# Kernel tuning notes

Hardware: AMD Instinct MI355X
Metric: run time of the kernel (lower is better)

Reference implementation:

```python
import jax, jax.numpy as jnp
import numpy as np

B, N, D, H = 4, 16384, 256, 2
EPS_LN = 1e-5
EPS_NORM = 1e-12


def _layernorm(x, w, b):
    # WithBias_LayerNorm over last dim (biased variance)
    mu = jnp.mean(x, axis=-1, keepdims=True)
    var = jnp.var(x, axis=-1, keepdims=True)
    return (x - mu) / jnp.sqrt(var + EPS_LN) * w + b


def _l2norm(x):
    # torch F.normalize along dim=-1
    n = jnp.sqrt(jnp.sum(x * x, axis=-1, keepdims=True))
    return x / jnp.maximum(n, EPS_NORM)


def setup_inputs() -> dict:
    key = jax.random.key(0)
    ks = jax.random.split(key, 8)
    s = 0.02
    return {
        "input_R": jax.random.normal(ks[0], (B, N, D), jnp.float32),
        "input_S": jax.random.normal(ks[1], (B, N, D), jnp.float32),
        "lnS_w": jnp.ones((D,), jnp.float32),
        "lnS_b": jnp.zeros((D,), jnp.float32),
        "lnR_w": jnp.ones((D,), jnp.float32),
        "lnR_b": jnp.zeros((D,), jnp.float32),
        "Wq": jax.random.normal(ks[2], (D, D), jnp.float32) * s,
        "bq": jax.random.normal(ks[3], (D,), jnp.float32) * s,
        "Wkv": jax.random.normal(ks[4], (2 * D, D), jnp.float32) * s,
        "bkv": jax.random.normal(ks[5], (2 * D,), jnp.float32) * s,
        "Wo": jax.random.normal(ks[6], (D, D), jnp.float32) * s,
        "bo": jax.random.normal(ks[7], (D,), jnp.float32) * s,
        "temperature": jnp.ones((H, 1, 1), jnp.float32),
    }


def reference(input_R, input_S, lnS_w, lnS_b, lnR_w, lnR_b,
              Wq, bq, Wkv, bkv, Wo, bo, temperature):
    b, n, d = input_S.shape
    h = temperature.shape[0]
    c = d // h
    # LayerNorm over channels, then permute to [b, d, n] (Conv1d layout)
    x = _layernorm(input_R, lnR_w, lnR_b).transpose(0, 2, 1)  # kv source
    y = _layernorm(input_S, lnS_w, lnS_b).transpose(0, 2, 1)  # q source
    # 1x1 conv == channel matmul
    kv = jnp.einsum('od,bdn->bon', Wkv, x) + bkv[None, :, None]  # [b,2d,n]
    k, v = jnp.split(kv, 2, axis=1)                              # [b,d,n]
    q = jnp.einsum('od,bdn->bon', Wq, y) + bq[None, :, None]     # [b,d,n]
    # split heads: [b, h, c, n]
    q = _l2norm(q.reshape(b, h, c, n))
    k = _l2norm(k.reshape(b, h, c, n))
    v = v.reshape(b, h, c, n)
    # channel attention: [b,h,c,c]
    attn = jnp.einsum('bhcn,bhdn->bhcd', q, k) * temperature[None]
    attn = jax.nn.softmax(attn, axis=-1)
    out = jnp.einsum('bhcd,bhdn->bhcn', attn, v).reshape(b, d, n)
    out = jnp.einsum('od,bdn->bon', Wo, out) + bo[None, :, None]
    return out.transpose(0, 2, 1)  # [b, n, d]
```

## Files before the change

### kernel.cpp

```cpp
#include <hip/hip_runtime.h>
#include <hip/hip_bf16.h>

typedef __attribute__((ext_vector_type(8))) short short8;
typedef __attribute__((ext_vector_type(4))) float f32x4;
typedef unsigned short u16;

#define DEVI static __device__ __forceinline__

constexpr int kB = 4;
constexpr int kN = 16384;
constexpr int kD = 256;
constexpr int kH = 2;
constexpr int kC = 128;

constexpr size_t SZ_T16 = (size_t)kB * kD * kN * 2;
constexpr size_t O_Yt   = 0;
constexpr size_t O_Xt   = O_Yt + SZ_T16;
constexpr size_t O_Xrow = O_Xt + SZ_T16;
constexpr size_t SZ_G   = (size_t)3 * kB * kD * kD * 4;
constexpr size_t O_G    = O_Xrow + SZ_T16;
constexpr size_t O_ysum = O_G + SZ_G;
constexpr size_t O_xsum = O_ysum + (size_t)kB * kD * 4;
constexpr size_t O_T    = O_xsum + (size_t)kB * kD * 4;
constexpr size_t O_qy   = O_T + SZ_G;
constexpr size_t O_kq   = O_qy + (size_t)kB * kD * 4;
constexpr size_t O_nq2  = O_kq + (size_t)kB * kD * 4;
constexpr size_t O_nk2  = O_nq2 + (size_t)kB * kD * 4;
constexpr size_t O_A    = O_nk2 + (size_t)kB * kD * 4;
constexpr size_t SZ_A   = (size_t)kB * kH * kC * kC * 4;
constexpr size_t O_W3   = O_A + SZ_A;
constexpr size_t O_b3   = O_W3 + (size_t)kB * kD * kD * 2;
constexpr size_t WS_NEED = O_b3 + (size_t)kB * kD * 4;

DEVI u16 f2bf(float x) {
    unsigned u = __builtin_bit_cast(unsigned, x);
    unsigned r = (u + 0x7FFFu + ((u >> 16) & 1u)) >> 16;
    return (u16)r;
}

DEVI void gload_lds16(const void* g, void* l) {
    __builtin_amdgcn_global_load_lds(
        (const __attribute__((address_space(1))) unsigned int*)g,
        (__attribute__((address_space(3))) unsigned int*)l, 16, 0, 0);
}

__global__ __launch_bounds__(256) void ln_kernel(
    const float* __restrict__ x, const float* __restrict__ w, const float* __restrict__ bia,
    u16* __restrict__ outT, u16* __restrict__ outR, float* __restrict__ colsum)
{
    constexpr int ROWS = 32;
    __shared__ u16 tile[256][36];
    __shared__ float csum[4][256];
    int blk = blockIdx.x;
    int b = blk >> 9;
    int n0 = (blk & 511) * ROWS;
    int lane = threadIdx.x & 63, wave = threadIdx.x >> 6;

    float wv[4], bv[4];
#pragma unroll
    for (int j = 0; j < 4; j++) { int c = lane + 64 * j; wv[j] = w[c]; bv[j] = bia[c]; }
    float acc[4] = {0.f, 0.f, 0.f, 0.f};

    for (int i = 0; i < 8; i++) {
        int r = wave * 8 + i;
        const float* xp = x + ((size_t)(b * kN + n0 + r)) * kD;
        float v[4];
#pragma unroll
        for (int j = 0; j < 4; j++) v[j] = xp[lane + 64 * j];
        float s  = v[0] + v[1] + v[2] + v[3];
        float sq = v[0]*v[0] + v[1]*v[1] + v[2]*v[2] + v[3]*v[3];
#pragma unroll
        for (int off = 32; off; off >>= 1) { s += __shfl_xor(s, off); sq += __shfl_xor(sq, off); }
        float mean = s * (1.f / kD);
        float var  = sq * (1.f / kD) - mean * mean;
        float rstd = rsqrtf(var + 1e-5f);
#pragma unroll
        for (int j = 0; j < 4; j++) {
            float y = (v[j] - mean) * rstd * wv[j] + bv[j];
            acc[j] += y;
            u16 u = f2bf(y);
            tile[lane + 64 * j][r] = u;
            if (outR) outR[((size_t)(b * kN + n0 + r)) * kD + lane + 64 * j] = u;
        }
    }
#pragma unroll
    for (int j = 0; j < 4; j++) csum[wave][lane + 64 * j] = acc[j];
    __syncthreads();
    int t = threadIdx.x;
    unsafeAtomicAdd(&colsum[b * kD + t], csum[0][t] + csum[1][t] + csum[2][t] + csum[3][t]);

#pragma unroll
    for (int pass = 0; pass < 2; pass++) {
        int c = pass * 128 + (t >> 1);
        int q = t & 1;
        const u16* src = &tile[c][q * 16];
        uint2 p0 = *(const uint2*)(src + 0);
        uint2 p1 = *(const uint2*)(src + 4);
        uint2 p2 = *(const uint2*)(src + 8);
        uint2 p3 = *(const uint2*)(src + 12);
        u16* dst = outT + ((size_t)(b * kD + c)) * kN + n0 + q * 16;
        *(uint4*)(dst)     = make_uint4(p0.x, p0.y, p1.x, p1.y);
        *(uint4*)(dst + 8) = make_uint4(p2.x, p2.y, p3.x, p3.y);
    }
}

__global__ __launch_bounds__(256) void gram_kernel(
    const u16* __restrict__ Yt, const u16* __restrict__ Xt, float* __restrict__ G)
{
    __shared__ __align__(16) char smem[32768];

    int id = blockIdx.x;
    int b = id / 192;
    int r = id % 192;
    int chunk = r / 12;
    int r2 = r % 12;
    int which = r2 >> 2;
    int tm = (r2 >> 1) & 1, tn = r2 & 1;
    const u16* Ap = (which == 2) ? Xt : Yt;
    const u16* Bp = (which == 1) ? Yt : Xt;

    int lane = threadIdx.x & 63, wave = threadIdx.x >> 6;
    int wr = wave >> 1, wc = wave & 1;
    int li = lane & 15, klo = lane >> 4;

    const u16* Abase = Ap + ((size_t)(b * kD + tm * 128)) * kN + (size_t)chunk * 1024;
    const u16* Bbase = Bp + ((size_t)(b * kD + tn * 128)) * kN + (size_t)chunk * 1024;
    const u16* gsrcA[4];
    const u16* gsrcB[4];
    char* ldst[4];
#pragma unroll
    for (int j = 0; j < 4; j++) {
        int u = (wave * 4 + j) * 64 + lane;
        int row = u >> 3;
        int sl = ((u & 7) ^ (row & 7)) * 8;
        gsrcA[j] = Abase + (size_t)row * kN + sl;
        gsrcB[j] = Bbase + (size_t)row * kN + sl;
        ldst[j] = smem + (wave * 4 + j) * 1024;
    }

    unsigned offA[2][4], offB[2][4];
#pragma unroll
    for (int kk = 0; kk < 2; kk++)
#pragma unroll
        for (int f = 0; f < 4; f++) {
            int rowA = wr * 64 + f * 16 + li;
            int rowB = wc * 64 + f * 16 + li;
            int e = kk * 32 + klo * 8;
            offA[kk][f] = rowA * 128 + ((e ^ ((rowA & 7) << 3)) * 2);
            offB[kk][f] = 16384 + rowB * 128 + ((e ^ ((rowB & 7) << 3)) * 2);
        }

    f32x4 acc[4][4] = {};
    for (int step = 0; step < 16; step++) {
#pragma unroll
        for (int j = 0; j < 4; j++) {
            gload_lds16(gsrcA[j] + step * 64, ldst[j]);
            gload_lds16(gsrcB[j] + step * 64, ldst[j] + 16384);
        }
        __syncthreads();
#pragma unroll
        for (int kk = 0; kk < 2; kk++) {
            short8 a[4], bb[4];
#pragma unroll
            for (int f = 0; f < 4; f++) a[f]  = *(const short8*)(smem + offA[kk][f]);
#pragma unroll
            for (int f = 0; f < 4; f++) bb[f] = *(const short8*)(smem + offB[kk][f]);
#pragma unroll
            for (int fi = 0; fi < 4; fi++)
#pragma unroll
                for (int fj = 0; fj < 4; fj++)
                    acc[fi][fj] = __builtin_amdgcn_mfma_f32_16x16x32_bf16(a[fi], bb[fj], acc[fi][fj], 0, 0, 0);
        }
        __syncthreads();
    }

    float* Gb = G + ((size_t)(which * 4 + b)) * (kD * kD);
#pragma unroll
    for (int fi = 0; fi < 4; fi++) {
        int row = tm * 128 + wr * 64 + fi * 16 + klo * 4;
#pragma unroll
        for (int fj = 0; fj < 4; fj++) {
            int col = tn * 128 + wc * 64 + fj * 16 + li;
#pragma unroll
            for (int rr = 0; rr < 4; rr++)
                unsafeAtomicAdd(&Gb[(size_t)(row + rr) * kD + col], acc[fi][fj][rr]);
        }
    }
}

__global__ __launch_bounds__(256) void tmul_kernel(
    const float* __restrict__ G, const float* __restrict__ Wq, const float* __restrict__ Wkv,
    float* __restrict__ T)
{
    int id = blockIdx.x;
    int otile = id & 31; id >>= 5;
    int b = id & 3;      id >>= 2;
    int which = id;
    const float* W  = (which == 2) ? Wkv : Wq;
    const float* Gb = G + ((size_t)(which * 4 + b)) * (kD * kD);
    float* Tb       = T + ((size_t)(which * 4 + b)) * (kD * kD);
    int d = threadIdx.x;
    int o0 = otile * 8;
    float acc[8] = {};
    for (int m = 0; m < 256; m++) {
        float g = Gb[(size_t)m * kD + d];
#pragma unroll
        for (int oo = 0; oo < 8; oo++) acc[oo] = fmaf(W[(o0 + oo) * kD + m], g, acc[oo]);
    }
#pragma unroll
    for (int oo = 0; oo < 8; oo++) Tb[(size_t)(o0 + oo) * kD + d] = acc[oo];
}

__global__ __launch_bounds__(256) void vec_kernel(
    const float* __restrict__ T, const float* __restrict__ Wq, const float* __restrict__ Wkv,
    const float* __restrict__ bq, const float* __restrict__ bkv,
    const float* __restrict__ ysum, const float* __restrict__ xsum,
    float* __restrict__ qy, float* __restrict__ kq,
    float* __restrict__ nq2, float* __restrict__ nk2)
{
    __shared__ float ys[256], xs[256];
    int b = blockIdx.x, e = threadIdx.x;
    ys[e] = ysum[b * kD + e];
    xs[e] = xsum[b * kD + e];
    __syncthreads();
    const float* T2  = T + ((size_t)(1 * 4 + b)) * (kD * kD) + (size_t)e * kD;
    const float* T3  = T + ((size_t)(2 * 4 + b)) * (kD * kD) + (size_t)e * kD;
    const float* wqr = Wq + (size_t)e * kD;
    const float* wkr = Wkv + (size_t)e * kD;
    float dqy = 0, dkq = 0, d2 = 0, d3 = 0;
    for (int m = 0; m < 256; m++) {
        float a = wqr[m], c = wkr[m];
        dqy = fmaf(a, ys[m], dqy);
        dkq = fmaf(c, xs[m], dkq);
        d2  = fmaf(T2[m], a, d2);
        d3  = fmaf(T3[m], c, d3);
    }
    float bqe = bq[e], bke = bkv[e];
    qy[b * kD + e] = dqy;
    kq[b * kD + e] = dkq;
    nq2[b * kD + e] = d2 + 2.f * bqe * dqy + (float)kN * bqe * bqe;
    nk2[b * kD + e] = d3 + 2.f * bke * dkq + (float)kN * bke * bke;
}

__global__ __launch_bounds__(128) void attn_kernel(
    const float* __restrict__ T, const float* __restrict__ Wkv,
    const float* __restrict__ bq, const float* __restrict__ bkv,
    const float* __restrict__ qy, const float* __restrict__ kq,
    const float* __restrict__ nq2, const float* __restrict__ nk2,
    const float* __restrict__ temperature, float* __restrict__ A)
{
    __shared__ float t1[256];
    __shared__ float red[4];
    int id = blockIdx.x;
    int c = id & 127; id >>= 7;
    int h = id & 1;
    int b = id >> 1;
    int e = h * 128 + c;
    int d = threadIdx.x;

    const float* T1 = T + ((size_t)(0 * 4 + b)) * (kD * kD) + (size_t)e * kD;
    t1[d] = T1[d];
    t1[128 + d] = T1[128 + d];
    __syncthreads();

    int f = h * 128 + d;
    const float* wkr = Wkv + (size_t)f * kD;
    float acc = 0;
    for (int m = 0; m < 256; m++) acc = fmaf(t1[m], wkr[m], acc);

    float bqe = bq[e], bkf = bkv[f];
    float graw = acc + bqe * kq[b * kD + f] + bkf * qy[b * kD + e] + (float)kN * bqe * bkf;
    float rq = 1.f / fmaxf(sqrtf(fmaxf(nq2[b * kD + e], 0.f)), 1e-12f);
    float rk = 1.f / fmaxf(sqrtf(fmaxf(nk2[b * kD + f], 0.f)), 1e-12f);
    float logit = graw * rq * rk * temperature[h];

    float mx = logit;
#pragma unroll
    for (int off = 32; off; off >>= 1) mx = fmaxf(mx, __shfl_xor(mx, off));
    int wv = d >> 6;
    if ((d & 63) == 0) red[wv] = mx;
    __syncthreads();
    mx = fmaxf(red[0], red[1]);
    float p = __expf(logit - mx);
    float sm = p;
#pragma unroll
    for (int off = 32; off; off >>= 1) sm += __shfl_xor(sm, off);
    if ((d & 63) == 0) red[2 + wv] = sm;
    __syncthreads();
    sm = red[2] + red[3];
    A[((size_t)((b * 2 + h) * kC + c)) * kC + d] = p / sm;
}

__global__ __launch_bounds__(256) void mmat_kernel(
    const float* __restrict__ A, const float* __restrict__ Wo,
    const float* __restrict__ Wkv, const float* __restrict__ bkv,
    const float* __restrict__ bo, u16* __restrict__ W3, float* __restrict__ b3)
{
    __shared__ float Ml[256];
    int id = blockIdx.x;
    int o = id & 255;
    int b = id >> 8;
    int t = threadIdx.x;
    int h = t >> 7, d = t & 127;

    const float* Ab  = A + ((size_t)(b * 2 + h)) * (kC * kC);
    const float* wor = Wo + (size_t)o * kD + h * 128;
    float acc = 0;
    for (int c2 = 0; c2 < 128; c2++) acc = fmaf(wor[c2], Ab[(size_t)c2 * kC + d], acc);
    Ml[t] = acc;
    __syncthreads();

    const float* wvp = Wkv + (size_t)256 * kD;
    float w3 = 0, bsum = 0;
    for (int e2 = 0; e2 < 256; e2++) {
        float m = Ml[e2];
        w3   = fmaf(m, wvp[(size_t)e2 * kD + t], w3);
        bsum = fmaf(m, bkv[256 + e2], bsum);
    }
    W3[((size_t)(b * kD + o)) * kD + t] = f2bf(w3);
    if (t == 0) b3[b * kD + o] = bsum + bo[o];
}

__global__ __launch_bounds__(256) void outgemm_kernel(
    const u16* __restrict__ Xrow, const u16* __restrict__ W3,
    const float* __restrict__ b3, float* __restrict__ out)
{
    __shared__ __align__(16) char smem[32768];

    int id = blockIdx.x;
    int ntile = id & 1;  id >>= 1;
    int mtile = id & 127; id >>= 7;
    int b = id;
    int lane = threadIdx.x & 63, wave = threadIdx.x >> 6;
    int wr = wave >> 1, wc = wave & 1;
    int li = lane & 15, klo = lane >> 4;

    const u16* Abase = Xrow + ((size_t)(b * kN + mtile * 128)) * kD;
    const u16* Bbase = W3 + ((size_t)(b * kD + ntile * 128)) * kD;
    const u16* gsrcA[4];
    const u16* gsrcB[4];
    char* ldst[4];
#pragma unroll
    for (int j = 0; j < 4; j++) {
        int u = (wave * 4 + j) * 64 + lane;
        int row = u >> 3;
        int sl = ((u & 7) ^ (row & 7)) * 8;
        gsrcA[j] = Abase + (size_t)row * kD + sl;
        gsrcB[j] = Bbase + (size_t)row * kD + sl;
        ldst[j] = smem + (wave * 4 + j) * 1024;
    }
    unsigned offA[2][4], offB[2][4];
#pragma unroll
    for (int kk = 0; kk < 2; kk++)
#pragma unroll
        for (int f = 0; f < 4; f++) {
            int rowA = wr * 64 + f * 16 + li;
            int rowB = wc * 64 + f * 16 + li;
            int e = kk * 32 + klo * 8;
            offA[kk][f] = rowA * 128 + ((e ^ ((rowA & 7) << 3)) * 2);
            offB[kk][f] = 16384 + rowB * 128 + ((e ^ ((rowB & 7) << 3)) * 2);
        }

    f32x4 acc[4][4] = {};
    for (int step = 0; step < 4; step++) {
#pragma unroll
        for (int j = 0; j < 4; j++) {
            gload_lds16(gsrcA[j] + step * 64, ldst[j]);
            gload_lds16(gsrcB[j] + step * 64, ldst[j] + 16384);
        }
        __syncthreads();
#pragma unroll
        for (int kk = 0; kk < 2; kk++) {
            short8 a[4], bb[4];
#pragma unroll
            for (int f = 0; f < 4; f++) a[f]  = *(const short8*)(smem + offA[kk][f]);
#pragma unroll
            for (int f = 0; f < 4; f++) bb[f] = *(const short8*)(smem + offB[kk][f]);
#pragma unroll
            for (int fi = 0; fi < 4; fi++)
#pragma unroll
                for (int fj = 0; fj < 4; fj++)
                    acc[fi][fj] = __builtin_amdgcn_mfma_f32_16x16x32_bf16(a[fi], bb[fj], acc[fi][fj], 0, 0, 0);
        }
        __syncthreads();
    }

    int n0 = mtile * 128 + wr * 64;
    int o0 = ntile * 128 + wc * 64;
#pragma unroll
    for (int fj = 0; fj < 4; fj++) {
        float bias = b3[b * kD + o0 + fj * 16 + li];
#pragma unroll
        for (int fi = 0; fi < 4; fi++) {
            int nr = n0 + fi * 16 + klo * 4;
#pragma unroll
            for (int rr = 0; rr < 4; rr++)
                out[((size_t)(b * kN + nr + rr)) * kD + o0 + fj * 16 + li] = acc[fi][fj][rr] + bias;
        }
    }
}

extern "C" void kernel_launch(void* const* d_in, const int* in_sizes, int n_in,
                              void* d_out, int out_size, void* d_ws, size_t ws_size,
                              hipStream_t stream)
{
    const float* input_R = (const float*)d_in[0];
    const float* input_S = (const float*)d_in[1];
    const float* lnS_w   = (const float*)d_in[2];
    const float* lnS_b   = (const float*)d_in[3];
    const float* lnR_w   = (const float*)d_in[4];
    const float* lnR_b   = (const float*)d_in[5];
    const float* Wq      = (const float*)d_in[6];
    const float* bq      = (const float*)d_in[7];
    const float* Wkv     = (const float*)d_in[8];
    const float* bkv     = (const float*)d_in[9];
    const float* Wo      = (const float*)d_in[10];
    const float* bo      = (const float*)d_in[11];
    const float* temp    = (const float*)d_in[12];
    float* out = (float*)d_out;
    char* ws = (char*)d_ws;

    u16*   Yt   = (u16*)(ws + O_Yt);
    u16*   Xt   = (u16*)(ws + O_Xt);
    u16*   Xrow = (u16*)(ws + O_Xrow);
    float* G    = (float*)(ws + O_G);
    float* ysum = (float*)(ws + O_ysum);
    float* xsum = (float*)(ws + O_xsum);
    float* T    = (float*)(ws + O_T);
    float* qy   = (float*)(ws + O_qy);
    float* kq   = (float*)(ws + O_kq);
    float* nq2  = (float*)(ws + O_nq2);
    float* nk2  = (float*)(ws + O_nk2);
    float* A    = (float*)(ws + O_A);
    u16*   W3   = (u16*)(ws + O_W3);
    float* b3   = (float*)(ws + O_b3);

    hipMemsetAsync(ws + O_G, 0, SZ_G + (size_t)2 * kB * kD * 4, stream);

    ln_kernel<<<2048, 256, 0, stream>>>(input_S, lnS_w, lnS_b, Yt, nullptr, ysum);
    ln_kernel<<<2048, 256, 0, stream>>>(input_R, lnR_w, lnR_b, Xt, Xrow, xsum);
    gram_kernel<<<768, 256, 0, stream>>>(Yt, Xt, G);
    tmul_kernel<<<384, 256, 0, stream>>>(G, Wq, Wkv, T);
    vec_kernel<<<4, 256, 0, stream>>>(T, Wq, Wkv, bq, bkv, ysum, xsum, qy, kq, nq2, nk2);
    attn_kernel<<<1024, 128, 0, stream>>>(T, Wkv, bq, bkv, qy, kq, nq2, nk2, temp, A);
    mmat_kernel<<<1024, 256, 0, stream>>>(A, Wo, Wkv, bkv, bo, W3, b3);
    outgemm_kernel<<<1024, 256, 0, stream>>>(Xrow, W3, b3, out);
}
```

Measured before the change: 440.8 us.

## Double-buffer LDS in gram and output GEMMs; parallelize vec_kernel across more blocks

The gram and output GEMM kernels now use two 32KB LDS buffers, so the next K-step's global-to-LDS loads are issued before computing on the current buffer, overlapping memory latency with MFMA work and removing one barrier per step. The vec_kernel is split from 4 blocks to 64, with 16 lanes cooperating on each dot product via shuffle reductions, instead of one thread looping over 256 elements. The larger LDS footprint may reduce the number of blocks resident per CU.

```diff
diff --git a/kernel.cpp b/kernel.cpp
--- a/kernel.cpp
+++ b/kernel.cpp
@@ -107,7 +107,7 @@
 __global__ __launch_bounds__(256) void gram_kernel(
     const u16* __restrict__ Yt, const u16* __restrict__ Xt, float* __restrict__ G)
 {
-    __shared__ __align__(16) char smem[32768];
+    __shared__ __align__(16) char smem[65536];
 
     int id = blockIdx.x;
     int b = id / 192;
@@ -127,7 +127,7 @@
     const u16* Bbase = Bp + ((size_t)(b * kD + tn * 128)) * kN + (size_t)chunk * 1024;
     const u16* gsrcA[4];
     const u16* gsrcB[4];
-    char* ldst[4];
+    unsigned lofs[4];
 #pragma unroll
     for (int j = 0; j < 4; j++) {
         int u = (wave * 4 + j) * 64 + lane;
@@ -135,7 +135,7 @@
         int sl = ((u & 7) ^ (row & 7)) * 8;
         gsrcA[j] = Abase + (size_t)row * kN + sl;
         gsrcB[j] = Bbase + (size_t)row * kN + sl;
-        ldst[j] = smem + (wave * 4 + j) * 1024;
+        lofs[j] = (wave * 4 + j) * 1024;
     }
 
     unsigned offA[2][4], offB[2][4];
@@ -151,28 +151,42 @@
         }
 
     f32x4 acc[4][4] = {};
-    for (int step = 0; step < 16; step++) {
+
+    auto STAGE = [&](int buf, int step) {
 #pragma unroll
         for (int j = 0; j < 4; j++) {
-            gload_lds16(gsrcA[j] + step * 64, ldst[j]);
-            gload_lds16(gsrcB[j] + step * 64, ldst[j] + 16384);
-        }
-        __syncthreads();
+            char* l = smem + (buf << 15) + lofs[j];
+            gload_lds16(gsrcA[j] + step * 64, l);
+            gload_lds16(gsrcB[j] + step * 64, l + 16384);
+        }
+    };
+    auto COMPUTE = [&](int buf) {
+        const char* base = smem + (buf << 15);
 #pragma unroll
         for (int kk = 0; kk < 2; kk++) {
             short8 a[4], bb[4];
 #pragma unroll
-            for (int f = 0; f < 4; f++) a[f]  = *(const short8*)(smem + offA[kk][f]);
-#pragma unroll
-            for (int f = 0; f < 4; f++) bb[f] = *(const short8*)(smem + offB[kk][f]);
+            for (int f = 0; f < 4; f++) a[f]  = *(const short8*)(base + offA[kk][f]);
+#pragma unroll
+            for (int f = 0; f < 4; f++) bb[f] = *(const short8*)(base + offB[kk][f]);
 #pragma unroll
             for (int fi = 0; fi < 4; fi++)
 #pragma unroll
                 for (int fj = 0; fj < 4; fj++)
                     acc[fi][fj] = __builtin_amdgcn_mfma_f32_16x16x32_bf16(a[fi], bb[fj], acc[fi][fj], 0, 0, 0);
         }
+    };
+
+    STAGE(0, 0);
+    __syncthreads();
+    int cur = 0;
+    for (int step = 0; step < 15; step++) {
+        STAGE(cur ^ 1, step + 1);
+        COMPUTE(cur);
         __syncthreads();
-    }
+        cur ^= 1;
+    }
+    COMPUTE(cur);
 
     float* Gb = G + ((size_t)(which * 4 + b)) * (kD * kD);
 #pragma unroll
@@ -219,27 +233,42 @@
     float* __restrict__ nq2, float* __restrict__ nk2)
 {
     __shared__ float ys[256], xs[256];
-    int b = blockIdx.x, e = threadIdx.x;
-    ys[e] = ysum[b * kD + e];
-    xs[e] = xsum[b * kD + e];
-    __syncthreads();
+    int blk = blockIdx.x;
+    int b = blk >> 4, eg = blk & 15;
+    int t = threadIdx.x;
+    ys[t] = ysum[b * kD + t];
+    xs[t] = xsum[b * kD + t];
+    __syncthreads();
+    int el = t >> 4, ml = t & 15;
+    int e = eg * 16 + el;
     const float* T2  = T + ((size_t)(1 * 4 + b)) * (kD * kD) + (size_t)e * kD;
     const float* T3  = T + ((size_t)(2 * 4 + b)) * (kD * kD) + (size_t)e * kD;
     const float* wqr = Wq + (size_t)e * kD;
     const float* wkr = Wkv + (size_t)e * kD;
     float dqy = 0, dkq = 0, d2 = 0, d3 = 0;
-    for (int m = 0; m < 256; m++) {
+#pragma unroll
+    for (int i = 0; i < 16; i++) {
+        int m = i * 16 + ml;
         float a = wqr[m], c = wkr[m];
         dqy = fmaf(a, ys[m], dqy);
         dkq = fmaf(c, xs[m], dkq);
         d2  = fmaf(T2[m], a, d2);
         d3  = fmaf(T3[m], c, d3);
     }
-    float bqe = bq[e], bke = bkv[e];
-    qy[b * kD + e] = dqy;
-    kq[b * kD + e] = dkq;
-    nq2[b * kD + e] = d2 + 2.f * bqe * dqy + (float)kN * bqe * bqe;
-    nk2[b * kD + e] = d3 + 2.f * bke * dkq + (float)kN * bke * bke;
+#pragma unroll
+    for (int off = 8; off; off >>= 1) {
+        dqy += __shfl_xor(dqy, off);
+        dkq += __shfl_xor(dkq, off);
+        d2  += __shfl_xor(d2, off);
+        d3  += __shfl_xor(d3, off);
+    }
+    if (ml == 0) {
+        float bqe = bq[e], bke = bkv[e];
+        qy[b * kD + e] = dqy;
+        kq[b * kD + e] = dkq;
+        nq2[b * kD + e] = d2 + 2.f * bqe * dqy + (float)kN * bqe * bqe;
+        nk2[b * kD + e] = d3 + 2.f * bke * dkq + (float)kN * bke * bke;
+    }
 }
 
 __global__ __launch_bounds__(128) void attn_kernel(
@@ -325,7 +354,7 @@
     const u16* __restrict__ Xrow, const u16* __restrict__ W3,
     const float* __restrict__ b3, float* __restrict__ out)
 {
-    __shared__ __align__(16) char smem[32768];
+    __shared__ __align__(16) char smem[65536];
 
     int id = blockIdx.x;
     int ntile = id & 1;  id >>= 1;
@@ -339,7 +368,7 @@
     const u16* Bbase = W3 + ((size_t)(b * kD + ntile * 128)) * kD;
     const u16* gsrcA[4];
     const u16* gsrcB[4];
-    char* ldst[4];
+    unsigned lofs[4];
 #pragma unroll
     for (int j = 0; j < 4; j++) {
         int u = (wave * 4 + j) * 64 + lane;
@@ -347,7 +376,7 @@
         int sl = ((u & 7) ^ (row & 7)) * 8;
         gsrcA[j] = Abase + (size_t)row * kD + sl;
         gsrcB[j] = Bbase + (size_t)row * kD + sl;
-        ldst[j] = smem + (wave * 4 + j) * 1024;
+        lofs[j] = (wave * 4 + j) * 1024;
     }
     unsigned offA[2][4], offB[2][4];
 #pragma unroll
@@ -362,28 +391,42 @@
         }
 
     f32x4 acc[4][4] = {};
-    for (int step = 0; step < 4; step++) {
+
+    auto STAGE = [&](int buf, int step) {
 #pragma unroll
         for (int j = 0; j < 4; j++) {
-            gload_lds16(gsrcA[j] + step * 64, ldst[j]);
-            gload_lds16(gsrcB[j] + step * 64, ldst[j] + 16384);
-        }
-        __syncthreads();
+            char* l = smem + (buf << 15) + lofs[j];
+            gload_lds16(gsrcA[j] + step * 64, l);
+            gload_lds16(gsrcB[j] + step * 64, l + 16384);
+        }
+    };
+    auto COMPUTE = [&](int buf) {
+        const char* base = smem + (buf << 15);
 #pragma unroll
         for (int kk = 0; kk < 2; kk++) {
             short8 a[4], bb[4];
 #pragma unroll
-            for (int f = 0; f < 4; f++) a[f]  = *(const short8*)(smem + offA[kk][f]);
-#pragma unroll
-            for (int f = 0; f < 4; f++) bb[f] = *(const short8*)(smem + offB[kk][f]);
+            for (int f = 0; f < 4; f++) a[f]  = *(const short8*)(base + offA[kk][f]);
+#pragma unroll
+            for (int f = 0; f < 4; f++) bb[f] = *(const short8*)(base + offB[kk][f]);
 #pragma unroll
             for (int fi = 0; fi < 4; fi++)
 #pragma unroll
                 for (int fj = 0; fj < 4; fj++)
                     acc[fi][fj] = __builtin_amdgcn_mfma_f32_16x16x32_bf16(a[fi], bb[fj], acc[fi][fj], 0, 0, 0);
         }
+    };
+
+    STAGE(0, 0);
+    __syncthreads();
+    int cur = 0;
+    for (int step = 0; step < 3; step++) {
+        STAGE(cur ^ 1, step + 1);
+        COMPUTE(cur);
         __syncthreads();
-    }
+        cur ^= 1;
+    }
+    COMPUTE(cur);
 
     int n0 = mtile * 128 + wr * 64;
     int o0 = ntile * 128 + wc * 64;
@@ -441,7 +484,7 @@
     ln_kernel<<<2048, 256, 0, stream>>>(input_R, lnR_w, lnR_b, Xt, Xrow, xsum);
     gram_kernel<<<768, 256, 0, stream>>>(Yt, Xt, G);
     tmul_kernel<<<384, 256, 0, stream>>>(G, Wq, Wkv, T);
-    vec_kernel<<<4, 256, 0, stream>>>(T, Wq, Wkv, bq, bkv, ysum, xsum, qy, kq, nq2, nk2);
+    vec_kernel<<<64, 256, 0, stream>>>(T, Wq, Wkv, bq, bkv, ysum, xsum, qy, kq, nq2, nk2);
     attn_kernel<<<1024, 128, 0, stream>>>(T, Wkv, bq, bkv, qy, kq, nq2, nk2, temp, A);
     mmat_kernel<<<1024, 256, 0, stream>>>(A, Wo, Wkv, bkv, bo, W3, b3);
     outgemm_kernel<<<1024, 256, 0, stream>>>(Xrow, W3, b3, out);
```

New measurement: 400.0 us. -9.3%, faster.
